# Performance work log

Hardware: AMD Instinct MI355X
Metric: run time of the kernel (lower is better)

## Reference

```python
import jax, jax.numpy as jnp
import numpy as np

H = 16  # n_head

def _rotate_half(x):
    d = x.shape[-1] // 2
    return jnp.concatenate([-x[..., d:], x[..., :d]], axis=-1)

def setup_inputs() -> dict:
    key = jax.random.key(0)
    ks = jax.random.split(key, 12)
    b, t, f, h = 8, 1024, 1024, H
    d = f // h
    inp = {
        "query": jax.random.normal(ks[0], (b, t, f), jnp.float32),
        "key": jax.random.normal(ks[1], (b, t, f), jnp.float32),
        "value": jax.random.normal(ks[2], (b, t, f), jnp.float32),
    }
    # realistic rotary cos/sin, shape (t,1,1,d_k)
    inv_freq = 1.0 / (10000.0 ** (np.arange(0, d, 2, dtype=np.float32) / d))
    pos = np.arange(t, dtype=np.float32)[:, None] * inv_freq[None, :]  # (t, d/2)
    emb = np.concatenate([pos, pos], axis=-1)  # (t, d)
    inp["cos"] = jnp.asarray(np.cos(emb)).reshape(t, 1, 1, d)
    inp["sin"] = jnp.asarray(np.sin(emb)).reshape(t, 1, 1, d)
    inp["mask"] = jax.random.randint(ks[3], (b, t, t), 0, 2) > 0
    s = 1.0 / np.sqrt(f)
    inp["Wq"] = jax.random.normal(ks[4], (f, f), jnp.float32) * s
    inp["bq"] = jax.random.normal(ks[5], (f,), jnp.float32) * 0.02
    inp["Wk"] = jax.random.normal(ks[6], (f, f), jnp.float32) * s
    inp["bk"] = jax.random.normal(ks[7], (f,), jnp.float32) * 0.02
    inp["Wv"] = jax.random.normal(ks[8], (f, f), jnp.float32) * s
    inp["bv"] = jax.random.normal(ks[9], (f,), jnp.float32) * 0.02
    inp["Wo"] = jax.random.normal(ks[10], (f, f), jnp.float32) * s
    inp["bo"] = jax.random.normal(ks[11], (f,), jnp.float32) * 0.02
    return inp

def reference(query, key, value, cos, sin, mask, Wq, bq, Wk, bk, Wv, bv, Wo, bo):
    b, t, f = query.shape
    h = H
    d = f // h
    # RoPE applied pre-projection, per-head layout (b,t,h,d)
    c = cos.reshape(1, t, 1, d)  # broadcast over batch and heads
    s = sin.reshape(1, t, 1, d)
    qr = query.reshape(b, t, h, d)
    kr = key.reshape(b, t, h, d)
    qr = qr * c + _rotate_half(qr) * s
    kr = kr * c + _rotate_half(kr) * s
    q_in = qr.reshape(b, t, f)
    k_in = kr.reshape(b, t, f)
    # QKV projections (nn.Linear: x @ W.T + b), then split heads -> (b,h,t,d)
    q = (jnp.einsum('btf,gf->btg', q_in, Wq) + bq).reshape(b, t, h, d).transpose(0, 2, 1, 3)
    k = (jnp.einsum('btf,gf->btg', k_in, Wk) + bk).reshape(b, t, h, d).transpose(0, 2, 1, 3)
    v = (jnp.einsum('btf,gf->btg', value, Wv) + bv).reshape(b, t, h, d).transpose(0, 2, 1, 3)
    scores = jnp.einsum('bhqd,bhkd->bhqk', q, k) / jnp.sqrt(jnp.asarray(d, q.dtype))
    m = mask[:, None, :, :]  # (b,1,t,t)
    scores = jnp.where(m, jnp.asarray(-10000.0, scores.dtype), scores)
    attn = jax.nn.softmax(scores, axis=-1)
    attn = jnp.where(m, jnp.asarray(0.0, attn.dtype), attn)
    out = jnp.einsum('bhqk,bhkd->bhqd', attn, v)  # (b,h,t,d)
    out = out.transpose(0, 2, 1, 3).reshape(b, t, f)
    return jnp.einsum('btf,gf->btg', out, Wo) + bo
```

## Files before the change

kernel.cpp:

```cpp
#include <hip/hip_runtime.h>
#include <stdint.h>

typedef short short8 __attribute__((ext_vector_type(8)));
typedef float f32x4 __attribute__((ext_vector_type(4)));
typedef unsigned short ushort4v __attribute__((ext_vector_type(4)));
typedef unsigned int uint4v __attribute__((ext_vector_type(4)));
typedef unsigned long long u64;

#if __has_builtin(__builtin_amdgcn_exp2f)
#define EXP2(x) __builtin_amdgcn_exp2f(x)
#else
#define EXP2(x) exp2f(x)
#endif

__device__ __forceinline__ unsigned perm_hi16(unsigned hi, unsigned lo) {
#if __has_builtin(__builtin_amdgcn_perm)
  return __builtin_amdgcn_perm(hi, lo, 0x07060302u);
#else
  return (hi & 0xffff0000u) | (lo >> 16);
#endif
}

__device__ __forceinline__ unsigned short f2bf(float f) {
  union { float f; unsigned u; } v; v.f = f;
  unsigned r = v.u + 0x7fffu + ((v.u >> 16) & 1u);
  return (unsigned short)(r >> 16);
}

__device__ __forceinline__ unsigned cvt_pk_bf16(float lo, float hi) {
  unsigned r;
  asm("v_cvt_pk_bf16_f32 %0, %1, %2" : "=v"(r) : "v"(lo), "v"(hi));
  return r;
}

__device__ __forceinline__ void gld_lds16(const void* g, void* l) {
  __builtin_amdgcn_global_load_lds((const __attribute__((address_space(1))) void*)g,
                                   (__attribute__((address_space(3))) void*)l, 16, 0, 0);
}

__global__ void mask_pack(const int* __restrict__ mask, u64* __restrict__ bits) {
  const int tid = blockIdx.x * 256 + threadIdx.x;
  const int w = tid >> 6, j = tid & 63;
  const int gh = w & 1, ktb = (w >> 1) & 7, bq = w >> 4;
  const int nt = (j >> 2) & 7, r = j & 3, g = gh * 2 + (j >> 5);
  const int k = nt * 16 + g * 4 + r;
  const int v = mask[(size_t)bq * 1024 + ktb * 128 + k];
  const u64 b = __ballot(v != 0);
  if (j == 0) bits[w] = b;
}

__global__ void rope_kernel(const float* __restrict__ q, const float* __restrict__ k,
                            const float* __restrict__ cs, const float* __restrict__ sn,
                            unsigned short* __restrict__ qo, unsigned short* __restrict__ ko) {
  const int idx = blockIdx.x * 256 + threadIdx.x;
  const int p   = idx & 7;
  const int bth = idx >> 3;
  const int t   = (bth >> 4) & 1023;
  const size_t base = (size_t)bth * 64;
  const int dd0 = p * 4;

  const float4 x0 = *(const float4*)(q + base + dd0);
  const float4 x1 = *(const float4*)(q + base + dd0 + 32);
  const float4 y0 = *(const float4*)(k + base + dd0);
  const float4 y1 = *(const float4*)(k + base + dd0 + 32);
  const float4 c0 = *(const float4*)(cs + t * 64 + dd0);
  const float4 c1 = *(const float4*)(cs + t * 64 + dd0 + 32);
  const float4 s0 = *(const float4*)(sn + t * 64 + dd0);
  const float4 s1 = *(const float4*)(sn + t * 64 + dd0 + 32);

  ushort4v qlo, qhi, klo, khi;
  qlo[0]=f2bf(x0.x*c0.x - x1.x*s0.x); qlo[1]=f2bf(x0.y*c0.y - x1.y*s0.y);
  qlo[2]=f2bf(x0.z*c0.z - x1.z*s0.z); qlo[3]=f2bf(x0.w*c0.w - x1.w*s0.w);
  qhi[0]=f2bf(x1.x*c1.x + x0.x*s1.x); qhi[1]=f2bf(x1.y*c1.y + x0.y*s1.y);
  qhi[2]=f2bf(x1.z*c1.z + x0.z*s1.z); qhi[3]=f2bf(x1.w*c1.w + x0.w*s1.w);
  klo[0]=f2bf(y0.x*c0.x - y1.x*s0.x); klo[1]=f2bf(y0.y*c0.y - y1.y*s0.y);
  klo[2]=f2bf(y0.z*c0.z - y1.z*s0.z); klo[3]=f2bf(y0.w*c0.w - y1.w*s0.w);
  khi[0]=f2bf(y1.x*c1.x + y0.x*s1.x); khi[1]=f2bf(y1.y*c1.y + y0.y*s1.y);
  khi[2]=f2bf(y1.z*c1.z + y0.z*s1.z); khi[3]=f2bf(y1.w*c1.w + y0.w*s1.w);

  *(ushort4v*)(qo + base + dd0)      = qlo;
  *(ushort4v*)(qo + base + dd0 + 32) = qhi;
  *(ushort4v*)(ko + base + dd0)      = klo;
  *(ushort4v*)(ko + base + dd0 + 32) = khi;
}

__global__ void cast_kernel(const float* __restrict__ src, unsigned short* __restrict__ dst, int n4) {
  const int i = blockIdx.x * 256 + threadIdx.x;
  if (i < n4) {
    const float4 v = *(const float4*)(src + (size_t)i * 4);
    ushort4v o;
    o[0]=f2bf(v.x); o[1]=f2bf(v.y); o[2]=f2bf(v.z); o[3]=f2bf(v.w);
    *(ushort4v*)(dst + (size_t)i * 4) = o;
  }
}

__global__ void cast4_kernel(const float* __restrict__ s0, const float* __restrict__ s1,
                             const float* __restrict__ s2, const float* __restrict__ s3,
                             unsigned short* __restrict__ d0, unsigned short* __restrict__ d1,
                             unsigned short* __restrict__ d2, unsigned short* __restrict__ d3) {
  const int m = blockIdx.y;
  const float* src = (m == 0) ? s0 : (m == 1) ? s1 : (m == 2) ? s2 : s3;
  unsigned short* dst = (m == 0) ? d0 : (m == 1) ? d1 : (m == 2) ? d2 : d3;
  const int i = blockIdx.x * 256 + threadIdx.x;
  const float4 v = *(const float4*)(src + (size_t)i * 4);
  ushort4v o;
  o[0]=f2bf(v.x); o[1]=f2bf(v.y); o[2]=f2bf(v.z); o[3]=f2bf(v.w);
  *(ushort4v*)(dst + (size_t)i * 4) = o;
}

template <int MODE>
__global__ __launch_bounds__(256, 2) void gemm_bt(
    const unsigned short* __restrict__ A, const unsigned short* __restrict__ Bw,
    const float* __restrict__ bias, void* __restrict__ C, float scale) {
  constexpr int K = 1024, N = 1024;
  const int tid = threadIdx.x;
  const int wave = tid >> 6, lane = tid & 63;
  const int m0 = blockIdx.x * 128, n0 = blockIdx.y * 128;
  __shared__ unsigned short Asm[128 * 64];
  __shared__ unsigned short Bsm[128 * 64];
  f32x4 acc[4][4] = {};
  const int wr = (wave >> 1) * 64, wc = (wave & 1) * 64;
  const int ld_row = lane >> 3;
  const int ld_col = ((lane & 7) ^ ld_row) * 8;
  const int fr = lane & 15, g = lane >> 4;
  const int fr7 = fr & 7;

  for (int k0 = 0; k0 < K; k0 += 64) {
#pragma unroll
    for (int j = 0; j < 4; ++j) {
      const int c = j * 4 + wave;
      gld_lds16(A  + (size_t)(m0 + 8 * c + ld_row) * K + k0 + ld_col, &Asm[c * 512]);
      gld_lds16(Bw + (size_t)(n0 + 8 * c + ld_row) * K + k0 + ld_col, &Bsm[c * 512]);
    }
    __syncthreads();
#pragma unroll
    for (int ks = 0; ks < 2; ++ks) {
      const int ch = ((ks * 4 + g) ^ fr7) * 8;
      short8 af[4], bf[4];
#pragma unroll
      for (int i = 0; i < 4; ++i)
        af[i] = *(const short8*)&Asm[(wr + i * 16 + fr) * 64 + ch];
#pragma unroll
      for (int i = 0; i < 4; ++i)
        bf[i] = *(const short8*)&Bsm[(wc + i * 16 + fr) * 64 + ch];
#pragma unroll
      for (int i = 0; i < 4; ++i)
#pragma unroll
        for (int j = 0; j < 4; ++j)
          acc[i][j] = __builtin_amdgcn_mfma_f32_16x16x32_bf16(af[i], bf[j], acc[i][j], 0, 0, 0);
    }
    __syncthreads();
  }

#pragma unroll
  for (int i = 0; i < 4; ++i) {
    const int row_base = m0 + wr + i * 16 + g * 4;
#pragma unroll
    for (int j = 0; j < 4; ++j) {
      const int col = n0 + wc + j * 16 + fr;
      const float bval = bias[col];
      if (MODE == 0) {
        float* Co = (float*)C;
#pragma unroll
        for (int r = 0; r < 4; ++r)
          Co[(size_t)(row_base + r) * N + col] = (acc[i][j][r] + bval) * scale;
      } else if (MODE == 1) {
        unsigned short* Co = (unsigned short*)C;
        const int h_i = col >> 6, dd = col & 63;
#pragma unroll
        for (int r = 0; r < 4; ++r) {
          const int row = row_base + r;
          const int b_i = row >> 10, t_i = row & 1023;
          Co[((size_t)(b_i * 16 + h_i) * 1024 + t_i) * 64 + dd] = f2bf((acc[i][j][r] + bval) * scale);
        }
      } else {
        unsigned short* Co = (unsigned short*)C;
        const int h_i = col >> 6, dd = col & 63;
#pragma unroll
        for (int r = 0; r < 4; ++r) {
          const int row = row_base + r;
          const int b_i = row >> 10, t_i = row & 1023;
          const int kk = t_i & 127;
          const int kp = ((kk >> 4) & 3) * 32 + ((kk >> 2) & 3) * 8 + ((kk >> 6) & 1) * 4 + (kk & 3);
          Co[((size_t)(b_i * 16 + h_i) * 64 + dd) * 1024 + (t_i & ~127) + kp] =
              f2bf((acc[i][j][r] + bval) * scale);
        }
      }
    }
  }
}

__global__ __launch_bounds__(256, 2) void flash_attn(
    const unsigned short* __restrict__ Qp, const unsigned short* __restrict__ Kp,
    const unsigned short* __restrict__ Vp, const u64* __restrict__ mbits,
    unsigned short* __restrict__ O) {
  const int bh = blockIdx.x & 127, b_i = bh >> 4, h_i = bh & 15;
  const int q0 = (blockIdx.x >> 7) * 128;
  const int tid = threadIdx.x, wave = tid >> 6, lane = tid & 63;
  const unsigned short* Qb = Qp + (size_t)bh * 65536;
  const unsigned short* Kb = Kp + (size_t)bh * 65536;
  const unsigned short* Vb = Vp + (size_t)bh * 65536;
  const u64* mb = mbits + (size_t)b_i * 16384;

  __shared__ unsigned short smem[16384];
  unsigned short* Vsm = smem;
  unsigned short* Ksm = smem + 8192;

  const int fr = lane & 15, g = lane >> 4, fr7 = fr & 7;
  const int qw = q0 + wave * 32;

  short8 qf[2][2];
#pragma unroll
  for (int mt = 0; mt < 2; ++mt)
#pragma unroll
    for (int ks = 0; ks < 2; ++ks)
      qf[mt][ks] = *(const short8*)&Qb[(size_t)(qw + mt * 16 + fr) * 64 + ks * 32 + g * 8];

  f32x4 o_acc[2][4] = {};
  float l_run[2] = {0.0f, 0.0f};

  const int kld_row = lane >> 3;
  const int kld_col = ((lane & 7) ^ kld_row) * 8;
  const int vld_row = lane >> 4;
  const int vld_r7w = 4 * (wave & 1) + vld_row;
  const int vld_col = ((lane & 15) ^ vld_r7w) * 8;

  for (int kt = 0; kt < 1024; kt += 128) {
#pragma unroll
    for (int j = 0; j < 4; ++j) {
      const int c = j * 4 + wave;
      gld_lds16(Kb + (size_t)(kt + 8 * c + kld_row) * 64 + kld_col, &Ksm[c * 512]);
      gld_lds16(Vb + (size_t)(4 * c + vld_row) * 1024 + kt + vld_col, &Vsm[c * 512]);
    }
    __syncthreads();

    f32x4 s_acc[2][8] = {};
#pragma unroll
    for (int ks = 0; ks < 2; ++ks) {
      const int ch = ((ks * 4 + g) ^ fr7) * 8;
      short8 kf[8];
#pragma unroll
      for (int nt = 0; nt < 8; ++nt)
        kf[nt] = *(const short8*)&Ksm[(nt * 16 + fr) * 64 + ch];
      __builtin_amdgcn_s_setprio(1);
#pragma unroll
      for (int mt = 0; mt < 2; ++mt)
#pragma unroll
        for (int nt = 0; nt < 8; ++nt)
          s_acc[mt][nt] = __builtin_amdgcn_mfma_f32_16x16x32_bf16(kf[nt], qf[mt][ks], s_acc[mt][nt], 0, 0, 0);
      __builtin_amdgcn_s_setprio(0);
    }

    short8 pf[2][4];
#pragma unroll
    for (int mt = 0; mt < 2; ++mt) {
      const u64 w = mb[(size_t)(qw + mt * 16 + fr) * 16 + (kt >> 7) * 2 + (g >> 1)];
      const unsigned bits = (unsigned)(w >> ((g & 1) * 32));
      float lp = l_run[mt];
#pragma unroll
      for (int ks2 = 0; ks2 < 4; ++ks2) {
        float e[8];
#pragma unroll
        for (int r = 0; r < 4; ++r) {
          float a = EXP2(s_acc[mt][ks2][r]);
          a = (bits & (1u << (ks2 * 4 + r))) ? 0.0f : a;
          float b2 = EXP2(s_acc[mt][ks2 + 4][r]);
          b2 = (bits & (1u << (16 + ks2 * 4 + r))) ? 0.0f : b2;
          e[r] = a; e[4 + r] = b2;
          lp += a + b2;
        }
        uint4v pk;
        pk[0] = cvt_pk_bf16(e[0], e[1]);
        pk[1] = cvt_pk_bf16(e[2], e[3]);
        pk[2] = cvt_pk_bf16(e[4], e[5]);
        pk[3] = cvt_pk_bf16(e[6], e[7]);
        union { uint4v u; short8 s; } cv; cv.u = pk;
        pf[mt][ks2] = cv.s;
      }
      l_run[mt] = lp;
    }

#pragma unroll
    for (int ks2 = 0; ks2 < 4; ++ks2) {
      const int cc = (ks2 * 4 + g) ^ fr7;
      short8 vf[4];
#pragma unroll
      for (int dt = 0; dt < 4; ++dt)
        vf[dt] = *(const short8*)&Vsm[(dt * 16 + fr) * 128 + cc * 8];
      __builtin_amdgcn_s_setprio(1);
#pragma unroll
      for (int mt = 0; mt < 2; ++mt)
#pragma unroll
        for (int dt = 0; dt < 4; ++dt)
          o_acc[mt][dt] = __builtin_amdgcn_mfma_f32_16x16x32_bf16(pf[mt][ks2], vf[dt], o_acc[mt][dt], 0, 0, 0);
      __builtin_amdgcn_s_setprio(0);
    }
    __syncthreads();
  }

#pragma unroll
  for (int mt = 0; mt < 2; ++mt) {
    float red = l_run[mt];
    red += __shfl_xor(red, 16);
    red += __shfl_xor(red, 32);
#pragma unroll
    for (int r = 0; r < 4; ++r) {
      const float lv = __shfl(red, g * 4 + r);
      const float inv_l = 1.0f / lv;
      const int qrow = qw + mt * 16 + g * 4 + r;
#pragma unroll
      for (int dt = 0; dt < 4; ++dt) {
        const int dcol = dt * 16 + fr;
        O[((size_t)(b_i * 1024 + qrow)) * 1024 + h_i * 64 + dcol] = f2bf(o_acc[mt][dt][r] * inv_l);
      }
    }
  }
}

extern "C" void kernel_launch(void* const* d_in, const int* in_sizes, int n_in,
                              void* d_out, int out_size, void* d_ws, size_t ws_size,
                              hipStream_t stream) {
  const float* query = (const float*)d_in[0];
  const float* key   = (const float*)d_in[1];
  const float* value = (const float*)d_in[2];
  const float* cosb  = (const float*)d_in[3];
  const float* sinb  = (const float*)d_in[4];
  const int*   mask  = (const int*)d_in[5];
  const float* Wq = (const float*)d_in[6];
  const float* bq = (const float*)d_in[7];
  const float* Wk = (const float*)d_in[8];
  const float* bk = (const float*)d_in[9];
  const float* Wv = (const float*)d_in[10];
  const float* bv = (const float*)d_in[11];
  const float* Wo = (const float*)d_in[12];
  const float* bo = (const float*)d_in[13];
  (void)in_sizes; (void)n_in; (void)out_size; (void)ws_size;

  char* ws = (char*)d_ws;
  const size_t MB = 1024 * 1024;
  unsigned short* q_in = (unsigned short*)(ws);
  unsigned short* k_in = (unsigned short*)(ws + 16 * MB);
  unsigned short* v_bf = (unsigned short*)(ws + 32 * MB);
  unsigned short* Qp   = (unsigned short*)(ws + 48 * MB);
  unsigned short* Kp   = (unsigned short*)(ws + 64 * MB);
  unsigned short* Vp   = (unsigned short*)(ws + 80 * MB);
  unsigned short* Wqb  = (unsigned short*)(ws + 96 * MB);
  unsigned short* Wkb  = (unsigned short*)(ws + 98 * MB);
  unsigned short* Wvb  = (unsigned short*)(ws + 100 * MB);
  unsigned short* Wob  = (unsigned short*)(ws + 102 * MB);
  u64*            mbits= (u64*)(ws + 104 * MB);
  unsigned short* attn = q_in;

  mask_pack<<<32768, 256, 0, stream>>>(mask, mbits);
  rope_kernel<<<4096, 256, 0, stream>>>(query, key, cosb, sinb, q_in, k_in);
  cast_kernel<<<8192, 256, 0, stream>>>(value, v_bf, 2097152);
  cast4_kernel<<<dim3(1024, 4), 256, 0, stream>>>(Wq, Wk, Wv, Wo, Wqb, Wkb, Wvb, Wob);

  dim3 g(64, 8), blk(256);
  gemm_bt<1><<<g, blk, 0, stream>>>(q_in, Wqb, bq, Qp, 0.18033688f);
  gemm_bt<1><<<g, blk, 0, stream>>>(k_in, Wkb, bk, Kp, 1.0f);
  gemm_bt<2><<<g, blk, 0, stream>>>(v_bf, Wvb, bv, Vp, 1.0f);
  flash_attn<<<1024, blk, 0, stream>>>(Qp, Kp, Vp, mbits, attn);
  gemm_bt<0><<<g, blk, 0, stream>>>(attn, Wob, bo, d_out, 1.0f);
}
```

Measured before the change: 343.3 us.

## Batch QKV GEMMs into one launch, fuse V cast into RoPE, MFMA row-sum

Merges the Q, K and V projection GEMMs into one grid-z-indexed kernel with a higher occupancy hint, and folds the value bf16 cast into the RoPE kernel, cutting launches and raising the number of concurrent blocks. In flash attention the softmax denominator is now accumulated by an extra MFMA against a ones vector instead of scalar adds plus cross-lane shuffles. The extra MFMA adds matrix-core work per tile, and the denominator is now summed from bf16-rounded probabilities, which changes rounding slightly.

After: 343.3 us. No clear change (+0.0%).

```diff
diff --git a/kernel.cpp b/kernel.cpp
--- a/kernel.cpp
+++ b/kernel.cpp
@@ -12,14 +12,6 @@
 #else
 #define EXP2(x) exp2f(x)
 #endif
-
-__device__ __forceinline__ unsigned perm_hi16(unsigned hi, unsigned lo) {
-#if __has_builtin(__builtin_amdgcn_perm)
-  return __builtin_amdgcn_perm(hi, lo, 0x07060302u);
-#else
-  return (hi & 0xffff0000u) | (lo >> 16);
-#endif
-}
 
 __device__ __forceinline__ unsigned short f2bf(float f) {
   union { float f; unsigned u; } v; v.f = f;
@@ -49,9 +41,11 @@
   if (j == 0) bits[w] = b;
 }
 
-__global__ void rope_kernel(const float* __restrict__ q, const float* __restrict__ k,
-                            const float* __restrict__ cs, const float* __restrict__ sn,
-                            unsigned short* __restrict__ qo, unsigned short* __restrict__ ko) {
+__global__ void rope_cast_kernel(const float* __restrict__ q, const float* __restrict__ k,
+                                 const float* __restrict__ v,
+                                 const float* __restrict__ cs, const float* __restrict__ sn,
+                                 unsigned short* __restrict__ qo, unsigned short* __restrict__ ko,
+                                 unsigned short* __restrict__ vo) {
   const int idx = blockIdx.x * 256 + threadIdx.x;
   const int p   = idx & 7;
   const int bth = idx >> 3;
@@ -82,16 +76,15 @@
   *(ushort4v*)(qo + base + dd0 + 32) = qhi;
   *(ushort4v*)(ko + base + dd0)      = klo;
   *(ushort4v*)(ko + base + dd0 + 32) = khi;
-}
-
-__global__ void cast_kernel(const float* __restrict__ src, unsigned short* __restrict__ dst, int n4) {
-  const int i = blockIdx.x * 256 + threadIdx.x;
-  if (i < n4) {
-    const float4 v = *(const float4*)(src + (size_t)i * 4);
-    ushort4v o;
-    o[0]=f2bf(v.x); o[1]=f2bf(v.y); o[2]=f2bf(v.z); o[3]=f2bf(v.w);
-    *(ushort4v*)(dst + (size_t)i * 4) = o;
-  }
+
+  const size_t vb = (size_t)idx * 8;
+  const float4 va = *(const float4*)(v + vb);
+  const float4 vbv = *(const float4*)(v + vb + 4);
+  ushort4v oa, ob;
+  oa[0]=f2bf(va.x); oa[1]=f2bf(va.y); oa[2]=f2bf(va.z); oa[3]=f2bf(va.w);
+  ob[0]=f2bf(vbv.x); ob[1]=f2bf(vbv.y); ob[2]=f2bf(vbv.z); ob[3]=f2bf(vbv.w);
+  *(ushort4v*)(vo + vb)     = oa;
+  *(ushort4v*)(vo + vb + 4) = ob;
 }
 
 __global__ void cast4_kernel(const float* __restrict__ s0, const float* __restrict__ s1,
@@ -108,10 +101,94 @@
   *(ushort4v*)(dst + (size_t)i * 4) = o;
 }
 
-template <int MODE>
-__global__ __launch_bounds__(256, 2) void gemm_bt(
+__global__ __launch_bounds__(256, 4) void gemm_qkv(
+    const unsigned short* __restrict__ Aq, const unsigned short* __restrict__ Ak,
+    const unsigned short* __restrict__ Av,
+    const unsigned short* __restrict__ Bq, const unsigned short* __restrict__ Bk,
+    const unsigned short* __restrict__ Bv,
+    const float* __restrict__ bq, const float* __restrict__ bk, const float* __restrict__ bv,
+    unsigned short* __restrict__ Cq, unsigned short* __restrict__ Ck,
+    unsigned short* __restrict__ Cv) {
+  constexpr int K = 1024;
+  const int z = blockIdx.z;
+  const unsigned short* A  = (z == 0) ? Aq : (z == 1) ? Ak : Av;
+  const unsigned short* Bw = (z == 0) ? Bq : (z == 1) ? Bk : Bv;
+  const float* bias        = (z == 0) ? bq : (z == 1) ? bk : bv;
+  unsigned short* Co       = (z == 0) ? Cq : (z == 1) ? Ck : Cv;
+  const float scale = (z == 0) ? 0.18033688f : 1.0f;
+
+  const int tid = threadIdx.x;
+  const int wave = tid >> 6, lane = tid & 63;
+  const int m0 = blockIdx.x * 128, n0 = blockIdx.y * 128;
+  __shared__ unsigned short Asm[128 * 64];
+  __shared__ unsigned short Bsm[128 * 64];
+  f32x4 acc[4][4] = {};
+  const int wr = (wave >> 1) * 64, wc = (wave & 1) * 64;
+  const int ld_row = lane >> 3;
+  const int ld_col = ((lane & 7) ^ ld_row) * 8;
+  const int fr = lane & 15, g = lane >> 4;
+  const int fr7 = fr & 7;
+
+  for (int k0 = 0; k0 < K; k0 += 64) {
+#pragma unroll
+    for (int j = 0; j < 4; ++j) {
+      const int c = j * 4 + wave;
+      gld_lds16(A  + (size_t)(m0 + 8 * c + ld_row) * K + k0 + ld_col, &Asm[c * 512]);
+      gld_lds16(Bw + (size_t)(n0 + 8 * c + ld_row) * K + k0 + ld_col, &Bsm[c * 512]);
+    }
+    __syncthreads();
+#pragma unroll
+    for (int ks = 0; ks < 2; ++ks) {
+      const int ch = ((ks * 4 + g) ^ fr7) * 8;
+      short8 af[4], bf[4];
+#pragma unroll
+      for (int i = 0; i < 4; ++i)
+        af[i] = *(const short8*)&Asm[(wr + i * 16 + fr) * 64 + ch];
+#pragma unroll
+      for (int i = 0; i < 4; ++i)
+        bf[i] = *(const short8*)&Bsm[(wc + i * 16 + fr) * 64 + ch];
+#pragma unroll
+      for (int i = 0; i < 4; ++i)
+#pragma unroll
+        for (int j = 0; j < 4; ++j)
+          acc[i][j] = __builtin_amdgcn_mfma_f32_16x16x32_bf16(af[i], bf[j], acc[i][j], 0, 0, 0);
+    }
+    __syncthreads();
+  }
+
+#pragma unroll
+  for (int i = 0; i < 4; ++i) {
+    const int row_base = m0 + wr + i * 16 + g * 4;
+#pragma unroll
+    for (int j = 0; j < 4; ++j) {
+      const int col = n0 + wc + j * 16 + fr;
+      const float bval = bias[col];
+      const int h_i = col >> 6, dd = col & 63;
+      if (z < 2) {
+#pragma unroll
+        for (int r = 0; r < 4; ++r) {
+          const int row = row_base + r;
+          const int b_i = row >> 10, t_i = row & 1023;
+          Co[((size_t)(b_i * 16 + h_i) * 1024 + t_i) * 64 + dd] = f2bf((acc[i][j][r] + bval) * scale);
+        }
+      } else {
+#pragma unroll
+        for (int r = 0; r < 4; ++r) {
+          const int row = row_base + r;
+          const int b_i = row >> 10, t_i = row & 1023;
+          const int kk = t_i & 127;
+          const int kp = ((kk >> 4) & 3) * 32 + ((kk >> 2) & 3) * 8 + ((kk >> 6) & 1) * 4 + (kk & 3);
+          Co[((size_t)(b_i * 16 + h_i) * 64 + dd) * 1024 + (t_i & ~127) + kp] =
+              f2bf((acc[i][j][r] + bval));
+        }
+      }
+    }
+  }
+}
+
+__global__ __launch_bounds__(256, 2) void gemm_o(
     const unsigned short* __restrict__ A, const unsigned short* __restrict__ Bw,
-    const float* __restrict__ bias, void* __restrict__ C, float scale) {
+    const float* __restrict__ bias, float* __restrict__ C) {
   constexpr int K = 1024, N = 1024;
   const int tid = threadIdx.x;
   const int wave = tid >> 6, lane = tid & 63;
@@ -159,33 +236,9 @@
     for (int j = 0; j < 4; ++j) {
       const int col = n0 + wc + j * 16 + fr;
       const float bval = bias[col];
-      if (MODE == 0) {
-        float* Co = (float*)C;
-#pragma unroll
-        for (int r = 0; r < 4; ++r)
-          Co[(size_t)(row_base + r) * N + col] = (acc[i][j][r] + bval) * scale;
-      } else if (MODE == 1) {
-        unsigned short* Co = (unsigned short*)C;
-        const int h_i = col >> 6, dd = col & 63;
-#pragma unroll
-        for (int r = 0; r < 4; ++r) {
-          const int row = row_base + r;
-          const int b_i = row >> 10, t_i = row & 1023;
-          Co[((size_t)(b_i * 16 + h_i) * 1024 + t_i) * 64 + dd] = f2bf((acc[i][j][r] + bval) * scale);
-        }
-      } else {
-        unsigned short* Co = (unsigned short*)C;
-        const int h_i = col >> 6, dd = col & 63;
-#pragma unroll
-        for (int r = 0; r < 4; ++r) {
-          const int row = row_base + r;
-          const int b_i = row >> 10, t_i = row & 1023;
-          const int kk = t_i & 127;
-          const int kp = ((kk >> 4) & 3) * 32 + ((kk >> 2) & 3) * 8 + ((kk >> 6) & 1) * 4 + (kk & 3);
-          Co[((size_t)(b_i * 16 + h_i) * 64 + dd) * 1024 + (t_i & ~127) + kp] =
-              f2bf((acc[i][j][r] + bval) * scale);
-        }
-      }
+#pragma unroll
+      for (int r = 0; r < 4; ++r)
+        C[(size_t)(row_base + r) * N + col] = acc[i][j][r] + bval;
     }
   }
 }
@@ -217,7 +270,8 @@
       qf[mt][ks] = *(const short8*)&Qb[(size_t)(qw + mt * 16 + fr) * 64 + ks * 32 + g * 8];
 
   f32x4 o_acc[2][4] = {};
-  float l_run[2] = {0.0f, 0.0f};
+  f32x4 o_l[2] = {};
+  const short8 ones = {0x3F80, 0x3F80, 0x3F80, 0x3F80, 0x3F80, 0x3F80, 0x3F80, 0x3F80};
 
   const int kld_row = lane >> 3;
   const int kld_col = ((lane & 7) ^ kld_row) * 8;
@@ -256,7 +310,6 @@
     for (int mt = 0; mt < 2; ++mt) {
       const u64 w = mb[(size_t)(qw + mt * 16 + fr) * 16 + (kt >> 7) * 2 + (g >> 1)];
       const unsigned bits = (unsigned)(w >> ((g & 1) * 32));
-      float lp = l_run[mt];
 #pragma unroll
       for (int ks2 = 0; ks2 < 4; ++ks2) {
         float e[8];
@@ -267,7 +320,6 @@
           float b2 = EXP2(s_acc[mt][ks2 + 4][r]);
           b2 = (bits & (1u << (16 + ks2 * 4 + r))) ? 0.0f : b2;
           e[r] = a; e[4 + r] = b2;
-          lp += a + b2;
         }
         uint4v pk;
         pk[0] = cvt_pk_bf16(e[0], e[1]);
@@ -277,7 +329,6 @@
         union { uint4v u; short8 s; } cv; cv.u = pk;
         pf[mt][ks2] = cv.s;
       }
-      l_run[mt] = lp;
     }
 
 #pragma unroll
@@ -289,10 +340,12 @@
         vf[dt] = *(const short8*)&Vsm[(dt * 16 + fr) * 128 + cc * 8];
       __builtin_amdgcn_s_setprio(1);
 #pragma unroll
-      for (int mt = 0; mt < 2; ++mt)
+      for (int mt = 0; mt < 2; ++mt) {
 #pragma unroll
         for (int dt = 0; dt < 4; ++dt)
           o_acc[mt][dt] = __builtin_amdgcn_mfma_f32_16x16x32_bf16(pf[mt][ks2], vf[dt], o_acc[mt][dt], 0, 0, 0);
+        o_l[mt] = __builtin_amdgcn_mfma_f32_16x16x32_bf16(pf[mt][ks2], ones, o_l[mt], 0, 0, 0);
+      }
       __builtin_amdgcn_s_setprio(0);
     }
     __syncthreads();
@@ -300,13 +353,9 @@
 
 #pragma unroll
   for (int mt = 0; mt < 2; ++mt) {
-    float red = l_run[mt];
-    red += __shfl_xor(red, 16);
-    red += __shfl_xor(red, 32);
 #pragma unroll
     for (int r = 0; r < 4; ++r) {
-      const float lv = __shfl(red, g * 4 + r);
-      const float inv_l = 1.0f / lv;
+      const float inv_l = 1.0f / o_l[mt][r];
       const int qrow = qw + mt * 16 + g * 4 + r;
 #pragma unroll
       for (int dt = 0; dt < 4; ++dt) {
@@ -352,14 +401,12 @@
   unsigned short* attn = q_in;
 
   mask_pack<<<32768, 256, 0, stream>>>(mask, mbits);
-  rope_kernel<<<4096, 256, 0, stream>>>(query, key, cosb, sinb, q_in, k_in);
-  cast_kernel<<<8192, 256, 0, stream>>>(value, v_bf, 2097152);
+  rope_cast_kernel<<<4096, 256, 0, stream>>>(query, key, value, cosb, sinb, q_in, k_in, v_bf);
   cast4_kernel<<<dim3(1024, 4), 256, 0, stream>>>(Wq, Wk, Wv, Wo, Wqb, Wkb, Wvb, Wob);
 
-  dim3 g(64, 8), blk(256);
-  gemm_bt<1><<<g, blk, 0, stream>>>(q_in, Wqb, bq, Qp, 0.18033688f);
-  gemm_bt<1><<<g, blk, 0, stream>>>(k_in, Wkb, bk, Kp, 1.0f);
-  gemm_bt<2><<<g, blk, 0, stream>>>(v_bf, Wvb, bv, Vp, 1.0f);
+  dim3 blk(256);
+  gemm_qkv<<<dim3(64, 8, 3), blk, 0, stream>>>(q_in, k_in, v_bf, Wqb, Wkb, Wvb,
+                                               bq, bk, bv, Qp, Kp, Vp);
   flash_attn<<<1024, blk, 0, stream>>>(Qp, Kp, Vp, mbits, attn);
-  gemm_bt<0><<<g, blk, 0, stream>>>(attn, Wob, bo, d_out, 1.0f);
-}
+  gemm_o<<<dim3(64, 8), blk, 0, stream>>>(attn, Wob, bo, (float*)d_out);
+}
```
